# Kernel optimization log

Measured on AMD Instinct MI355X. Metric: run time of the kernel, lower is better.

Reference implementation:

```python
import jax, jax.numpy as jnp
import numpy as np

B, L, D = 8, 2048, 64

def setup_inputs() -> dict:
    key = jax.random.key(0)
    kq, kk, kv, kqm, kkm = jax.random.split(key, 5)
    return {
        "query": jax.random.normal(kq, (B, L, D), dtype=jnp.float32),
        "key": jax.random.normal(kk, (B, L, D), dtype=jnp.float32),
        "value": jax.random.normal(kv, (B, L, D), dtype=jnp.float32),
        "q_mask": jax.random.randint(kqm, (B, L), 0, 2, dtype=jnp.int32),
        "k_mask": jax.random.randint(kkm, (B, L), 0, 2, dtype=jnp.int32),
    }

def reference(query, key, value, q_mask, k_mask):
    # scale defaults to D_q; divide scores by sqrt(D_q)
    D_q = query.shape[-1]
    qm = q_mask.astype(jnp.float32)  # [B, L_q]
    km = k_mask.astype(jnp.float32)  # [B, L_k]
    # outer-product mask: [B, L_q, L_k]
    mask = qm[:, :, None] * km[:, None, :]
    scores = jnp.einsum("bqd,bkd->bqk", query, key) / jnp.sqrt(jnp.float32(D_q))
    # masked_fill(-inf).exp(): masked positions become exactly 0
    A = jnp.where(mask == 0, 0.0, jnp.exp(scores))  # [B, L_q, L_k]
    # sum clamped to min 1.0 (NOT a standard softmax normalization)
    A_sum = jnp.maximum(A.sum(axis=-1, keepdims=True), 1.0)
    attn = A / A_sum
    return jnp.einsum("bqk,bkd->bqd", attn, value)
```

## Files before the change

### kernel.cpp

```cpp
#include <hip/hip_runtime.h>
#include <hip/hip_bf16.h>
#include <stdint.h>

#define BB 8
#define LL 2048
#define DD 64

typedef short bf16x8 __attribute__((ext_vector_type(8)));
typedef float f32x4 __attribute__((ext_vector_type(4)));
typedef unsigned short ushort_t;
typedef __attribute__((address_space(1))) const unsigned int gas_u32;
typedef __attribute__((address_space(3))) unsigned int las_u32;

__device__ __forceinline__ unsigned pk2(float lo, float hi) {
    union { __hip_bfloat162 h; unsigned u; } c;
    c.h = __float22bfloat162_rn(make_float2(lo, hi));
    return c.u;
}
__device__ __forceinline__ float4 ld4(const float* __restrict__ p) {
    return *reinterpret_cast<const float4*>(p);
}
__device__ __forceinline__ bf16x8 cvt8f(float4 a, float4 b) {
    union { bf16x8 v; unsigned u[4]; } r;
    r.u[0] = pk2(a.x, a.y); r.u[1] = pk2(a.z, a.w);
    r.u[2] = pk2(b.x, b.y); r.u[3] = pk2(b.z, b.w);
    return r.v;
}
__device__ __forceinline__ void glds16(const void* g, void* lds_base_uniform) {
    __builtin_amdgcn_global_load_lds((gas_u32*)g, (las_u32*)lds_base_uniform, 16, 0, 0);
}
__device__ __forceinline__ float bfu2f(unsigned bits) {
    union { unsigned u; float f; } c; c.u = bits << 16; return c.f;
}
__device__ __forceinline__ unsigned f2bf_u(float f) {
    union { float f; unsigned u; } v; v.f = f;
    return (v.u + 0x8000u) >> 16;
}
__device__ __forceinline__ bf16x8 cvt8(const float* __restrict__ p) {
    float4 a = ld4(p), b = ld4(p + 4);
    union { bf16x8 v; unsigned u[4]; } r;
    r.u[0] = f2bf_u(a.x) | (f2bf_u(a.y) << 16);
    r.u[1] = f2bf_u(a.z) | (f2bf_u(a.w) << 16);
    r.u[2] = f2bf_u(b.x) | (f2bf_u(b.y) << 16);
    r.u[3] = f2bf_u(b.z) | (f2bf_u(b.w) << 16);
    return r.v;
}

__global__ __launch_bounds__(256) void pack_k_bf16(const float* __restrict__ K,
                                                   ushort_t* __restrict__ Kb) {
    size_t i = ((size_t)blockIdx.x * 256 + threadIdx.x) * 8;
    float4 a = ld4(K + i), b = ld4(K + i + 4);
    uint4 o = { pk2(a.x, a.y), pk2(a.z, a.w), pk2(b.x, b.y), pk2(b.z, b.w) };
    *reinterpret_cast<uint4*>(Kb + i) = o;
}

__global__ __launch_bounds__(256) void transpose_v_bf(const float* __restrict__ V,
                                                      ushort_t* __restrict__ VT) {
    __shared__ float t[64][65];
    const int b  = blockIdx.x >> 5;
    const int kt = (blockIdx.x & 31) << 6;
    {
        const int r  = threadIdx.x >> 2;
        const int cq = (threadIdx.x & 3) << 4;
        const float* src = V + ((size_t)(b * LL + kt + r)) * DD + cq;
        #pragma unroll
        for (int i = 0; i < 4; ++i) {
            float4 v = ld4(src + 4 * i);
            t[r][cq + 4 * i + 0] = v.x; t[r][cq + 4 * i + 1] = v.y;
            t[r][cq + 4 * i + 2] = v.z; t[r][cq + 4 * i + 3] = v.w;
        }
    }
    __syncthreads();
    {
        const int d  = threadIdx.x >> 2;
        const int kq = (threadIdx.x & 3) << 4;
        ushort_t* dst = VT + ((size_t)(b * DD + d)) * LL + kt + kq;
        #pragma unroll
        for (int u = 0; u < 2; ++u) {
            uint4 o;
            o.x = pk2(t[kq + 8 * u + 0][d], t[kq + 8 * u + 1][d]);
            o.y = pk2(t[kq + 8 * u + 2][d], t[kq + 8 * u + 3][d]);
            o.z = pk2(t[kq + 8 * u + 4][d], t[kq + 8 * u + 5][d]);
            o.w = pk2(t[kq + 8 * u + 6][d], t[kq + 8 * u + 7][d]);
            *reinterpret_cast<uint4*>(dst + 8 * u) = o;
        }
    }
}

__global__ __launch_bounds__(512, 4) void attn8(
    const float* __restrict__ Q,
    const ushort_t* __restrict__ Kbf,
    const ushort_t* __restrict__ VTb,
    const int* __restrict__ kmask,
    float* __restrict__ Opart)
{
    const int tid  = threadIdx.x;
    const int wave = tid >> 6;
    const int lane = tid & 63;
    const int ln   = lane & 15;
    const int quad = lane >> 4;

    const int bx    = blockIdx.x;
    const int ksp   = bx & 3;
    const int qt    = (bx >> 2) & 15;
    const int b     = bx >> 6;
    const int q0    = qt * 128;
    const int kbase = ksp * 512;

    __shared__ char     lds[2][16384];
    __shared__ ushort_t kmbf[512];

    const char* Kg = (const char*)Kbf + (size_t)b * LL * DD * 2;
    const char* Vg = (const char*)VTb + (size_t)b * DD * LL * 2;
    const int gr = tid >> 3;
    const int gc = (tid & 7) ^ (gr & 7);

    #define STAGE(buf, k0)                                                     \
        do {                                                                   \
            glds16(Kg + (size_t)(kbase + (k0) + gr) * 128 + gc * 16,           \
                   &lds[buf][wave * 1024]);                                    \
            glds16(Vg + (size_t)gr * (LL * 2) + (kbase + (k0)) * 2 + gc * 16,  \
                   &lds[buf][8192 + wave * 1024]);                             \
        } while (0)

    STAGE(0, 0);

    if (tid < 128) {
        int4 a = *reinterpret_cast<const int4*>(kmask + b * LL + kbase + tid * 4);
        uint2 u;
        u.x = (a.x ? 0x3F80u : 0u) | ((a.y ? 0x3F80u : 0u) << 16);
        u.y = (a.z ? 0x3F80u : 0u) | ((a.w ? 0x3F80u : 0u) << 16);
        *reinterpret_cast<uint2*>(kmbf + tid * 4) = u;
    }
    bf16x8 qf[2];
    {
        const float* qp = Q + ((size_t)(b * LL + q0 + 16 * wave + ln)) * DD + quad * 8;
        qf[0] = cvt8f(ld4(qp),      ld4(qp + 4));
        qf[1] = cvt8f(ld4(qp + 32), ld4(qp + 36));
    }

    f32x4 Oacc[4] = {{0,0,0,0},{0,0,0,0},{0,0,0,0},{0,0,0,0}};
    float dsum = 0.f;

    const int src0 = ln + ((quad & 1) << 5);
    const int src1 = src0 + 16;
    const bool hi  = quad >= 2;
    const float EC = 0.125f * 1.44269504f;

    for (int it = 0; it < 8; ++it) {
        __syncthreads();
        if (it != 7) STAGE((it + 1) & 1, (it + 1) * 64);

        const char* LK = lds[it & 1];
        const char* LV = lds[it & 1] + 8192;

        bf16x8 kf[4][2];
        #pragma unroll
        for (int tt = 0; tt < 4; ++tt) {
            const int r = 16 * tt + ln;
            #pragma unroll
            for (int dh = 0; dh < 2; ++dh) {
                const int c = (dh * 4 + quad) ^ (ln & 7);
                kf[tt][dh] = *reinterpret_cast<const bf16x8*>(LK + r * 128 + c * 16);
            }
        }
        bf16x8 vf[2][4];
        #pragma unroll
        for (int kh = 0; kh < 2; ++kh) {
            const int c = (kh * 4 + quad) ^ (ln & 7);
            #pragma unroll
            for (int db = 0; db < 4; ++db) {
                const int d = db * 16 + ln;
                vf[kh][db] = *reinterpret_cast<const bf16x8*>(LV + d * 128 + c * 16);
            }
        }

        unsigned w[4][2];
        #pragma unroll
        for (int tt = 0; tt < 4; ++tt) {
            f32x4 acc = (f32x4){0.f, 0.f, 0.f, 0.f};
            acc = __builtin_amdgcn_mfma_f32_16x16x32_bf16(kf[tt][0], qf[0], acc, 0, 0, 0);
            acc = __builtin_amdgcn_mfma_f32_16x16x32_bf16(kf[tt][1], qf[1], acc, 0, 0, 0);
            ushort4 mu = *reinterpret_cast<const ushort4*>(
                kmbf + it * 64 + 16 * tt + 4 * quad);
            float e0 = exp2f(acc[0] * EC) * bfu2f(mu.x);
            float e1 = exp2f(acc[1] * EC) * bfu2f(mu.y);
            float e2 = exp2f(acc[2] * EC) * bfu2f(mu.z);
            float e3 = exp2f(acc[3] * EC) * bfu2f(mu.w);
            dsum += (e0 + e1) + (e2 + e3);
            w[tt][0] = pk2(e0, e1);
            w[tt][1] = pk2(e2, e3);
        }
        #pragma unroll
        for (int g = 0; g < 2; ++g) {
            union { bf16x8 v; unsigned u[4]; } pf;
            unsigned a0 = __shfl(w[2*g][0], src0), b0 = __shfl(w[2*g+1][0], src0);
            unsigned a1 = __shfl(w[2*g][1], src0), b1 = __shfl(w[2*g+1][1], src0);
            unsigned a2 = __shfl(w[2*g][0], src1), b2 = __shfl(w[2*g+1][0], src1);
            unsigned a3 = __shfl(w[2*g][1], src1), b3 = __shfl(w[2*g+1][1], src1);
            pf.u[0] = hi ? b0 : a0;
            pf.u[1] = hi ? b1 : a1;
            pf.u[2] = hi ? b2 : a2;
            pf.u[3] = hi ? b3 : a3;
            #pragma unroll
            for (int db = 0; db < 4; ++db)
                Oacc[db] = __builtin_amdgcn_mfma_f32_16x16x32_bf16(pf.v, vf[g][db], Oacc[db], 0, 0, 0);
        }
    }
    #undef STAGE

    {
        float v = dsum;
        v += __shfl_xor(v, 16);
        v += __shfl_xor(v, 32);
        dsum = v;
    }

    float* pb = Opart + (size_t)bx * 8320;
    #pragma unroll
    for (int db = 0; db < 4; ++db)
        #pragma unroll
        for (int r = 0; r < 4; ++r)
            pb[(16 * wave + quad * 4 + r) * 64 + db * 16 + ln] = Oacc[db][r];
    if (quad == 0) pb[8192 + 16 * wave + ln] = dsum;
}

__global__ __launch_bounds__(256) void reduce_norm(
    const float* __restrict__ Opart,
    const int* __restrict__ qmask,
    float* __restrict__ Out)
{
    const int rb = blockIdx.x;
    const int qt = rb & 15;
    const int b  = rb >> 4;
    const int t  = threadIdx.x;
    const int q  = t >> 1;
    const int d0 = (t & 1) * 32;

    const float* p0 = Opart + (size_t)((b * 16 + qt) * 4 + 0) * 8320;
    const float* p1 = p0 + 8320;
    const float* p2 = p1 + 8320;
    const float* p3 = p2 + 8320;

    float dn = p0[8192 + q] + p1[8192 + q] + p2[8192 + q] + p3[8192 + q];
    float sc = qmask[b * LL + qt * 128 + q] ? (1.0f / fmaxf(dn, 1.0f)) : 0.0f;

    const int off = q * 64 + d0;
    float* op = Out + ((size_t)(b * LL + qt * 128 + q)) * DD + d0;
    #pragma unroll
    for (int i = 0; i < 8; ++i) {
        f32x4 v = *reinterpret_cast<const f32x4*>(p0 + off + 4 * i)
                + *reinterpret_cast<const f32x4*>(p1 + off + 4 * i)
                + *reinterpret_cast<const f32x4*>(p2 + off + 4 * i)
                + *reinterpret_cast<const f32x4*>(p3 + off + 4 * i);
        *reinterpret_cast<f32x4*>(op + 4 * i) = v * sc;
    }
}

__global__ __launch_bounds__(256, 4) void attn_mfma(
    const float* __restrict__ Q, const float* __restrict__ K,
    const float* __restrict__ V, const int* __restrict__ qmask,
    const int* __restrict__ kmask, float* __restrict__ Out)
{
    const int tid  = threadIdx.x;
    const int wave = tid >> 6;
    const int lane = tid & 63;
    const int n    = lane & 15;
    const int quad = lane >> 4;
    const int bx = blockIdx.x;
    const int b  = bx >> 7;
    const int q0 = (bx & 127) << 4;
    __shared__ float Pl[4][576];
    __shared__ float Opart2[4][16][68];
    __shared__ float Denp[4][16];
    const float* Qp = Q + ((size_t)(b * LL + q0 + n)) * DD + quad * 8;
    bf16x8 qf0 = cvt8(Qp);
    bf16x8 qf1 = cvt8(Qp + 32);
    const float* Kb = K + ((size_t)(b * LL) + n) * DD + quad * 8;
    const float* Vb = V + ((size_t)(b * LL) + quad * 8) * DD + n;
    const int* kmb = kmask + b * LL;
    f32x4 Oacc[4] = {{0,0,0,0},{0,0,0,0},{0,0,0,0},{0,0,0,0}};
    float den[4]  = {0.f, 0.f, 0.f, 0.f};
    float*       pw = &Pl[wave][144 * (n >> 3) + 36 * quad + (n & 7)];
    const float* pr = &Pl[wave][9 * lane];
    const int kbeg = wave * (LL / 4);
    const int kend = kbeg + (LL / 4);
    for (int k0 = kbeg; k0 < kend; k0 += 32) {
        const float* krow = Kb + (size_t)k0 * DD;
        bf16x8 kA0 = cvt8(krow);
        bf16x8 kA1 = cvt8(krow + 32);
        bf16x8 kB0 = cvt8(krow + 16 * DD);
        bf16x8 kB1 = cvt8(krow + 16 * DD + 32);
        f32x4 z = {0.f, 0.f, 0.f, 0.f};
        f32x4 S0 = __builtin_amdgcn_mfma_f32_16x16x32_bf16(qf0, kA0, z, 0, 0, 0);
        S0 = __builtin_amdgcn_mfma_f32_16x16x32_bf16(qf1, kA1, S0, 0, 0, 0);
        f32x4 S1 = __builtin_amdgcn_mfma_f32_16x16x32_bf16(qf0, kB0, z, 0, 0, 0);
        S1 = __builtin_amdgcn_mfma_f32_16x16x32_bf16(qf1, kB1, S1, 0, 0, 0);
        float km0 = (float)kmb[k0 + n];
        float km1 = (float)kmb[k0 + 16 + n];
        #pragma unroll
        for (int r = 0; r < 4; ++r) {
            float e0 = __expf(S0[r] * 0.125f) * km0;
            float e1 = __expf(S1[r] * 0.125f) * km1;
            den[r] += e0 + e1;
            pw[9 * r]       = e0;
            pw[288 + 9 * r] = e1;
        }
        __builtin_amdgcn_wave_barrier();
        float pv[8];
        #pragma unroll
        for (int j = 0; j < 8; ++j) pv[j] = pr[j];
        __builtin_amdgcn_wave_barrier();
        union { bf16x8 v; unsigned u[4]; } pf;
        #pragma unroll
        for (int j = 0; j < 4; ++j)
            pf.u[j] = f2bf_u(pv[2 * j]) | (f2bf_u(pv[2 * j + 1]) << 16);
        const float* vrow = Vb + (size_t)k0 * DD;
        #pragma unroll
        for (int db = 0; db < 4; ++db) {
            union { bf16x8 v; unsigned u[4]; } vfr;
            #pragma unroll
            for (int jj = 0; jj < 4; ++jj) {
                unsigned lo  = f2bf_u(vrow[(2 * jj) * DD + db * 16]);
                unsigned hi2 = f2bf_u(vrow[(2 * jj + 1) * DD + db * 16]);
                vfr.u[jj] = lo | (hi2 << 16);
            }
            Oacc[db] = __builtin_amdgcn_mfma_f32_16x16x32_bf16(pf.v, vfr.v, Oacc[db], 0, 0, 0);
        }
    }
    #pragma unroll
    for (int r = 0; r < 4; ++r) {
        float v = den[r];
        v += __shfl_xor(v, 1); v += __shfl_xor(v, 2);
        v += __shfl_xor(v, 4); v += __shfl_xor(v, 8);
        den[r] = v;
    }
    #pragma unroll
    for (int db = 0; db < 4; ++db)
        #pragma unroll
        for (int r = 0; r < 4; ++r)
            Opart2[wave][quad * 4 + r][db * 16 + n] = Oacc[db][r];
    if (n == 0) {
        #pragma unroll
        for (int r = 0; r < 4; ++r) Denp[wave][quad * 4 + r] = den[r];
    }
    __syncthreads();
    const int q  = tid >> 4;
    const int d0 = (tid & 15) * 4;
    f32x4 sum = *reinterpret_cast<const f32x4*>(&Opart2[0][q][d0]);
    sum += *reinterpret_cast<const f32x4*>(&Opart2[1][q][d0]);
    sum += *reinterpret_cast<const f32x4*>(&Opart2[2][q][d0]);
    sum += *reinterpret_cast<const f32x4*>(&Opart2[3][q][d0]);
    float dn  = Denp[0][q] + Denp[1][q] + Denp[2][q] + Denp[3][q];
    float inv = 1.0f / fmaxf(dn, 1.0f);
    float s   = qmask[b * LL + q0 + q] ? inv : 0.0f;
    f32x4 o   = sum * s;
    float* op = Out + ((size_t)(b * LL + q0 + q)) * DD + d0;
    *reinterpret_cast<f32x4*>(op) = o;
}

extern "C" void kernel_launch(void* const* d_in, const int* in_sizes, int n_in,
                              void* d_out, int out_size, void* d_ws, size_t ws_size,
                              hipStream_t stream) {
    (void)in_sizes; (void)n_in; (void)out_size;
    const float* Q  = (const float*)d_in[0];
    const float* K  = (const float*)d_in[1];
    const float* V  = (const float*)d_in[2];
    const int* qm   = (const int*)d_in[3];
    const int* km   = (const int*)d_in[4];
    float* Out      = (float*)d_out;

    const size_t elems   = (size_t)BB * LL * DD;
    const size_t part_off = 4u * 1024 * 1024;
    const size_t ws_need  = part_off + (size_t)512 * 8320 * sizeof(float);
    if (ws_size >= ws_need && d_ws != nullptr) {
        ushort_t* Kbf = (ushort_t*)d_ws;
        ushort_t* VTb = Kbf + elems;
        float* Opart  = (float*)((char*)d_ws + part_off);
        pack_k_bf16   <<<dim3(elems / (256 * 8)), dim3(256), 0, stream>>>(K, Kbf);
        transpose_v_bf<<<dim3(BB * (LL / 64)),    dim3(256), 0, stream>>>(V, VTb);
        attn8<<<dim3(512), dim3(512), 0, stream>>>(Q, Kbf, VTb, km, Opart);
        reduce_norm<<<dim3(128), dim3(256), 0, stream>>>(Opart, qm, Out);
    } else {
        attn_mfma<<<dim3(BB * (LL / 16)), dim3(256), 0, stream>>>(Q, K, V, qm, km, Out);
    }
}
```

Measured before the change: 105.7 us.

## Triple-buffer attention tiles, fuse prep kernels, use permlane swaps and setprio

Merges the K pack and V transpose kernels into one launch. The attention loop moves from a double to a triple LDS buffer with explicit vmcnt waits, so two tiles are in flight, and the Q and mask loads are issued before staging. The P-matrix shuffles are replaced by permlane32/16 swaps, the MFMA sections are wrapped in s_setprio, and the key mask is stored as float. The reduce kernel uses twice as many blocks. Together these aim to cut launch overhead, hide load latency and shorten the shuffle path, at the cost of more LDS and hand-placed waitcnts that are fragile.

```diff
diff --git a/kernel.cpp b/kernel.cpp
--- a/kernel.cpp
+++ b/kernel.cpp
@@ -28,9 +28,6 @@
 }
 __device__ __forceinline__ void glds16(const void* g, void* lds_base_uniform) {
     __builtin_amdgcn_global_load_lds((gas_u32*)g, (las_u32*)lds_base_uniform, 16, 0, 0);
-}
-__device__ __forceinline__ float bfu2f(unsigned bits) {
-    union { unsigned u; float f; } c; c.u = bits << 16; return c.f;
 }
 __device__ __forceinline__ unsigned f2bf_u(float f) {
     union { float f; unsigned u; } v; v.f = f;
@@ -46,19 +43,21 @@
     return r.v;
 }
 
-__global__ __launch_bounds__(256) void pack_k_bf16(const float* __restrict__ K,
-                                                   ushort_t* __restrict__ Kb) {
-    size_t i = ((size_t)blockIdx.x * 256 + threadIdx.x) * 8;
-    float4 a = ld4(K + i), b = ld4(K + i + 4);
-    uint4 o = { pk2(a.x, a.y), pk2(a.z, a.w), pk2(b.x, b.y), pk2(b.z, b.w) };
-    *reinterpret_cast<uint4*>(Kb + i) = o;
-}
-
-__global__ __launch_bounds__(256) void transpose_v_bf(const float* __restrict__ V,
-                                                      ushort_t* __restrict__ VT) {
+__global__ __launch_bounds__(256) void prep(const float* __restrict__ K,
+                                            const float* __restrict__ V,
+                                            ushort_t* __restrict__ Kb,
+                                            ushort_t* __restrict__ VT) {
     __shared__ float t[64][65];
-    const int b  = blockIdx.x >> 5;
-    const int kt = (blockIdx.x & 31) << 6;
+    if (blockIdx.x < 512) {
+        size_t i = ((size_t)blockIdx.x * 256 + threadIdx.x) * 8;
+        float4 a = ld4(K + i), b = ld4(K + i + 4);
+        uint4 o = { pk2(a.x, a.y), pk2(a.z, a.w), pk2(b.x, b.y), pk2(b.z, b.w) };
+        *reinterpret_cast<uint4*>(Kb + i) = o;
+        return;
+    }
+    const int bx = blockIdx.x - 512;
+    const int b  = bx >> 5;
+    const int kt = (bx & 31) << 6;
     {
         const int r  = threadIdx.x >> 2;
         const int cq = (threadIdx.x & 3) << 4;
@@ -107,8 +106,8 @@
     const int q0    = qt * 128;
     const int kbase = ksp * 512;
 
-    __shared__ char     lds[2][16384];
-    __shared__ ushort_t kmbf[512];
+    __shared__ char  lds[3][16384];
+    __shared__ float kmf[512];
 
     const char* Kg = (const char*)Kbf + (size_t)b * LL * DD * 2;
     const char* Vg = (const char*)VTb + (size_t)b * DD * LL * 2;
@@ -123,36 +122,32 @@
                    &lds[buf][8192 + wave * 1024]);                             \
         } while (0)
 
+    const float* qp = Q + ((size_t)(b * LL + q0 + 16 * wave + ln)) * DD + quad * 8;
+    float4 qa = ld4(qp), qb = ld4(qp + 4), qc = ld4(qp + 32), qd = ld4(qp + 36);
+    int4 km4 = {0, 0, 0, 0};
+    if (tid < 128)
+        km4 = *reinterpret_cast<const int4*>(kmask + b * LL + kbase + tid * 4);
+
     STAGE(0, 0);
-
+    STAGE(1, 64);
+
+    bf16x8 qf[2];
+    qf[0] = cvt8f(qa, qb);
+    qf[1] = cvt8f(qc, qd);
     if (tid < 128) {
-        int4 a = *reinterpret_cast<const int4*>(kmask + b * LL + kbase + tid * 4);
-        uint2 u;
-        u.x = (a.x ? 0x3F80u : 0u) | ((a.y ? 0x3F80u : 0u) << 16);
-        u.y = (a.z ? 0x3F80u : 0u) | ((a.w ? 0x3F80u : 0u) << 16);
-        *reinterpret_cast<uint2*>(kmbf + tid * 4) = u;
-    }
-    bf16x8 qf[2];
-    {
-        const float* qp = Q + ((size_t)(b * LL + q0 + 16 * wave + ln)) * DD + quad * 8;
-        qf[0] = cvt8f(ld4(qp),      ld4(qp + 4));
-        qf[1] = cvt8f(ld4(qp + 32), ld4(qp + 36));
-    }
+        float4 f = { km4.x ? 1.f : 0.f, km4.y ? 1.f : 0.f,
+                     km4.z ? 1.f : 0.f, km4.w ? 1.f : 0.f };
+        *reinterpret_cast<float4*>(kmf + tid * 4) = f;
+    }
+    asm volatile("s_waitcnt lgkmcnt(0)" ::: "memory");
 
     f32x4 Oacc[4] = {{0,0,0,0},{0,0,0,0},{0,0,0,0},{0,0,0,0}};
     float dsum = 0.f;
-
-    const int src0 = ln + ((quad & 1) << 5);
-    const int src1 = src0 + 16;
-    const bool hi  = quad >= 2;
     const float EC = 0.125f * 1.44269504f;
 
-    for (int it = 0; it < 8; ++it) {
-        __syncthreads();
-        if (it != 7) STAGE((it + 1) & 1, (it + 1) * 64);
-
-        const char* LK = lds[it & 1];
-        const char* LV = lds[it & 1] + 8192;
+    auto tile = [&](int cb_, int it_) {
+        const char* LK = lds[cb_];
+        const char* LV = lds[cb_] + 8192;
 
         bf16x8 kf[4][2];
         #pragma unroll
@@ -179,14 +174,16 @@
         #pragma unroll
         for (int tt = 0; tt < 4; ++tt) {
             f32x4 acc = (f32x4){0.f, 0.f, 0.f, 0.f};
+            __builtin_amdgcn_s_setprio(1);
             acc = __builtin_amdgcn_mfma_f32_16x16x32_bf16(kf[tt][0], qf[0], acc, 0, 0, 0);
             acc = __builtin_amdgcn_mfma_f32_16x16x32_bf16(kf[tt][1], qf[1], acc, 0, 0, 0);
-            ushort4 mu = *reinterpret_cast<const ushort4*>(
-                kmbf + it * 64 + 16 * tt + 4 * quad);
-            float e0 = exp2f(acc[0] * EC) * bfu2f(mu.x);
-            float e1 = exp2f(acc[1] * EC) * bfu2f(mu.y);
-            float e2 = exp2f(acc[2] * EC) * bfu2f(mu.z);
-            float e3 = exp2f(acc[3] * EC) * bfu2f(mu.w);
+            __builtin_amdgcn_s_setprio(0);
+            float4 mu = *reinterpret_cast<const float4*>(
+                kmf + it_ * 64 + 16 * tt + 4 * quad);
+            float e0 = exp2f(acc[0] * EC) * mu.x;
+            float e1 = exp2f(acc[1] * EC) * mu.y;
+            float e2 = exp2f(acc[2] * EC) * mu.z;
+            float e3 = exp2f(acc[3] * EC) * mu.w;
             dsum += (e0 + e1) + (e2 + e3);
             w[tt][0] = pk2(e0, e1);
             w[tt][1] = pk2(e2, e3);
@@ -194,19 +191,40 @@
         #pragma unroll
         for (int g = 0; g < 2; ++g) {
             union { bf16x8 v; unsigned u[4]; } pf;
-            unsigned a0 = __shfl(w[2*g][0], src0), b0 = __shfl(w[2*g+1][0], src0);
-            unsigned a1 = __shfl(w[2*g][1], src0), b1 = __shfl(w[2*g+1][1], src0);
-            unsigned a2 = __shfl(w[2*g][0], src1), b2 = __shfl(w[2*g+1][0], src1);
-            unsigned a3 = __shfl(w[2*g][1], src1), b3 = __shfl(w[2*g+1][1], src1);
-            pf.u[0] = hi ? b0 : a0;
-            pf.u[1] = hi ? b1 : a1;
-            pf.u[2] = hi ? b2 : a2;
-            pf.u[3] = hi ? b3 : a3;
+            #pragma unroll
+            for (int r = 0; r < 2; ++r) {
+                auto t32 = __builtin_amdgcn_permlane32_swap(
+                    w[2 * g][r], w[2 * g + 1][r], false, false);
+                auto t16 = __builtin_amdgcn_permlane16_swap(
+                    t32[0], t32[1], false, false);
+                pf.u[r]     = t16[0];
+                pf.u[r + 2] = t16[1];
+            }
+            __builtin_amdgcn_s_setprio(1);
             #pragma unroll
             for (int db = 0; db < 4; ++db)
-                Oacc[db] = __builtin_amdgcn_mfma_f32_16x16x32_bf16(pf.v, vf[g][db], Oacc[db], 0, 0, 0);
-        }
-    }
+                Oacc[db] = __builtin_amdgcn_mfma_f32_16x16x32_bf16(
+                    pf.v, vf[g][db], Oacc[db], 0, 0, 0);
+            __builtin_amdgcn_s_setprio(0);
+        }
+    };
+
+    int cb = 0;
+    for (int it = 0; it < 7; ++it) {
+        asm volatile("s_waitcnt vmcnt(2)" ::: "memory");
+        __builtin_amdgcn_s_barrier();
+        asm volatile("" ::: "memory");
+        if (it < 6) {
+            int sb = cb + 2; if (sb >= 3) sb -= 3;
+            STAGE(sb, (it + 2) * 64);
+        }
+        tile(cb, it);
+        cb = (cb == 2) ? 0 : cb + 1;
+    }
+    asm volatile("s_waitcnt vmcnt(0)" ::: "memory");
+    __builtin_amdgcn_s_barrier();
+    asm volatile("" ::: "memory");
+    tile(cb, 7);
     #undef STAGE
 
     {
@@ -230,12 +248,13 @@
     const int* __restrict__ qmask,
     float* __restrict__ Out)
 {
-    const int rb = blockIdx.x;
-    const int qt = rb & 15;
-    const int b  = rb >> 4;
-    const int t  = threadIdx.x;
-    const int q  = t >> 1;
-    const int d0 = (t & 1) * 32;
+    const int rb   = blockIdx.x;
+    const int half = rb & 1;
+    const int qt   = (rb >> 1) & 15;
+    const int b    = rb >> 5;
+    const int t    = threadIdx.x;
+    const int q    = half * 64 + (t >> 2);
+    const int d0   = (t & 3) * 16;
 
     const float* p0 = Opart + (size_t)((b * 16 + qt) * 4 + 0) * 8320;
     const float* p1 = p0 + 8320;
@@ -248,7 +267,7 @@
     const int off = q * 64 + d0;
     float* op = Out + ((size_t)(b * LL + qt * 128 + q)) * DD + d0;
     #pragma unroll
-    for (int i = 0; i < 8; ++i) {
+    for (int i = 0; i < 4; ++i) {
         f32x4 v = *reinterpret_cast<const f32x4*>(p0 + off + 4 * i)
                 + *reinterpret_cast<const f32x4*>(p1 + off + 4 * i)
                 + *reinterpret_cast<const f32x4*>(p2 + off + 4 * i)
@@ -377,10 +396,9 @@
         ushort_t* Kbf = (ushort_t*)d_ws;
         ushort_t* VTb = Kbf + elems;
         float* Opart  = (float*)((char*)d_ws + part_off);
-        pack_k_bf16   <<<dim3(elems / (256 * 8)), dim3(256), 0, stream>>>(K, Kbf);
-        transpose_v_bf<<<dim3(BB * (LL / 64)),    dim3(256), 0, stream>>>(V, VTb);
-        attn8<<<dim3(512), dim3(512), 0, stream>>>(Q, Kbf, VTb, km, Opart);
-        reduce_norm<<<dim3(128), dim3(256), 0, stream>>>(Opart, qm, Out);
+        prep       <<<dim3(768), dim3(256), 0, stream>>>(K, V, Kbf, VTb);
+        attn8      <<<dim3(512), dim3(512), 0, stream>>>(Q, Kbf, VTb, km, Opart);
+        reduce_norm<<<dim3(256), dim3(256), 0, stream>>>(Opart, qm, Out);
     } else {
         attn_mfma<<<dim3(BB * (LL / 16)), dim3(256), 0, stream>>>(Q, K, V, qm, km, Out);
     }
```

After: 100.3 us (median of 2 runs). -5.0%, faster.
